# Kernel optimization log

Hardware: AMD Instinct MI355X
Metric: run time of the kernel (lower is better)

Reference implementation:

```python
import jax, jax.numpy as jnp
import numpy as np

B, S, D, H = 2, 2048, 1024, 16
HD = D // H  # head_dim = 64
ROPE_BASE = 10000.0
INIT_STD = 0.02


def setup_inputs() -> dict:
    key = jax.random.key(0)
    k1, k2, k3 = jax.random.split(key, 3)
    x = jax.random.normal(k1, (B, S, D), dtype=jnp.float32)
    w_qkv = jax.random.normal(k2, (3 * D, D), dtype=jnp.float32) * INIT_STD
    w_out = jax.random.normal(k3, (D, D), dtype=jnp.float32) * (1.0 / np.sqrt(D))
    b_out = jnp.zeros((D,), dtype=jnp.float32)
    return {"x": x, "w_qkv": w_qkv, "w_out": w_out, "b_out": b_out}


def _rope_cos_sin(s_len, head_dim, dtype):
    theta = 1.0 / ROPE_BASE ** (jnp.arange(0, head_dim, 2, dtype=jnp.float32) / head_dim)
    freqs = jnp.outer(jnp.arange(s_len, dtype=jnp.float32), theta)  # [s, d/2]
    freqs = jnp.concatenate([freqs, freqs], axis=-1)  # [s, d]
    return jnp.cos(freqs).astype(dtype), jnp.sin(freqs).astype(dtype)


def _apply_rope(qk, cos, sin):
    # qk: [b, h, s, d]; rotate-half: (-x2, x1)
    d2 = qk.shape[-1] // 2
    x1, x2 = qk[..., :d2], qk[..., d2:]
    rot = jnp.concatenate([-x2, x1], axis=-1)
    return qk * cos + rot * sin


def reference(x, w_qkv, w_out, b_out):
    b, s, d = x.shape
    qkv = jnp.einsum('bsd,ed->bse', x, w_qkv)  # [b, s, 3D]
    qkv = qkv.reshape(b, s, 3 * H, HD).transpose(0, 2, 1, 3)  # [b, 3h, s, d]
    qk, v = qkv[:, :2 * H], qkv[:, 2 * H:]
    cos, sin = _rope_cos_sin(s, HD, x.dtype)
    qk = _apply_rope(qk, cos, sin)
    q, k = qk[:, :H], qk[:, H:]
    scale = 1.0 / np.sqrt(HD)
    scores = jnp.einsum('bhqd,bhkd->bhqk', q, k) * scale  # [b, h, s, s]
    causal = jnp.tril(jnp.ones((s, s), dtype=bool))
    scores = jnp.where(causal, scores, jnp.finfo(scores.dtype).min)
    attn = jax.nn.softmax(scores, axis=-1)
    o = jnp.einsum('bhqk,bhkd->bhqd', attn, v)  # [b, h, s, d]
    o = o.transpose(0, 2, 1, 3).reshape(b, s, d)
    return jnp.einsum('bsd,ed->bse', o, w_out) + b_out
```

## Files before the change

### kernel.cpp

```cpp
#include <hip/hip_runtime.h>
#include <hip/hip_fp16.h>
#include <math.h>

#define B_  2
#define S_  2048
#define D_  1024
#define H_  16
#define HD_ 64

typedef _Float16  f16;
typedef __attribute__((ext_vector_type(8))) _Float16 f16x8;
typedef __attribute__((ext_vector_type(4))) _Float16 f16x4;
typedef __attribute__((ext_vector_type(4))) float    f32x4;

#define LOG2E 1.4426950408889634f
#define L2_10000_DIV32 0.41524101186092029f
#define PS 72

__device__ __forceinline__ float fin(float v) { return (v == v) ? v : 0.0f; }

__device__ __forceinline__ f16x8 cvt8(const float* p) {
  float4 a = *(const float4*)p;
  float4 b = *(const float4*)(p + 4);
  f16x8 h;
  h[0] = (f16)a.x; h[1] = (f16)a.y; h[2] = (f16)a.z; h[3] = (f16)a.w;
  h[4] = (f16)b.x; h[5] = (f16)b.y; h[6] = (f16)b.z; h[7] = (f16)b.w;
  return h;
}

__global__ void __launch_bounds__(256)
k_qkv_rope(const float* __restrict__ x, const float* __restrict__ wqkv,
           f16* __restrict__ Qb, f16* __restrict__ Kb, f16* __restrict__ Vt)
{
  __shared__ __align__(16) f16 As[128 * 64];
  __shared__ __align__(16) f16 Bs[128 * 64];
  const int t = threadIdx.x;
  const int w = t >> 6;
  const int lane = t & 63;
  const int ll = lane & 15;
  const int quad = lane >> 4;
  const int wm = w >> 1, wn = w & 1;
  const int row0 = blockIdx.y * 128;
  const int col0 = blockIdx.x * 128;

  const f32x4 fz = {0.f, 0.f, 0.f, 0.f};
  f32x4 acc[4][4];
#pragma unroll
  for (int i = 0; i < 4; ++i)
#pragma unroll
    for (int j = 0; j < 4; ++j) acc[i][j] = fz;

  const int ldr = t >> 3;
  const int ldk = (t & 7) * 8;
  const float* ga = x    + (size_t)(row0 + ldr) * D_ + ldk;
  const float* gb = wqkv + (size_t)(col0 + ldr) * D_ + ldk;

  for (int kt = 0; kt < D_; kt += 64) {
    f16x8 ra[4], rb[4];
#pragma unroll
    for (int i = 0; i < 4; ++i) {
      ra[i] = cvt8(ga + (size_t)i * 32 * D_ + kt);
      rb[i] = cvt8(gb + (size_t)i * 32 * D_ + kt);
    }
    __syncthreads();
#pragma unroll
    for (int i = 0; i < 4; ++i) {
      *(f16x8*)&As[(i * 32 + ldr) * 64 + ldk] = ra[i];
      *(f16x8*)&Bs[(i * 32 + ldr) * 64 + ldk] = rb[i];
    }
    __syncthreads();
#pragma unroll
    for (int kk = 0; kk < 64; kk += 32) {
      f16x8 a[4], b[4];
#pragma unroll
      for (int mt = 0; mt < 4; ++mt)
        a[mt] = *(const f16x8*)&As[(wm * 64 + mt * 16 + ll) * 64 + kk + quad * 8];
#pragma unroll
      for (int nt = 0; nt < 4; ++nt)
        b[nt] = *(const f16x8*)&Bs[(wn * 64 + nt * 16 + ll) * 64 + kk + quad * 8];
#pragma unroll
      for (int mt = 0; mt < 4; ++mt)
#pragma unroll
        for (int nt = 0; nt < 4; ++nt)
          acc[mt][nt] = __builtin_amdgcn_mfma_f32_16x16x32_f16(
              a[mt], b[nt], acc[mt][nt], 0, 0, 0);
    }
  }

  const int h3 = (col0 >> 6) + wn;
  if (h3 < 32) {
    f16* dst = (h3 < 16) ? Qb : Kb;
    const int h = (h3 < 16) ? h3 : h3 - 16;
    const float th0 = exp2f(-(float)ll * L2_10000_DIV32);
    const float th1 = exp2f(-(float)(16 + ll) * L2_10000_DIV32);
#pragma unroll
    for (int mt = 0; mt < 4; ++mt) {
#pragma unroll
      for (int r = 0; r < 4; ++r) {
        const int row = row0 + wm * 64 + mt * 16 + quad * 4 + r;
        const int b = row >> 11;
        const int p = row & (S_ - 1);
        f16* base = dst + ((size_t)(b * H_ + h) * S_ + p) * HD_;
        const float fp = (float)p;
        float s0, c0, s1, c1;
        sincosf(fp * th0, &s0, &c0);
        sincosf(fp * th1, &s1, &c1);
        {
          float x1 = acc[mt][0][r], x2 = acc[mt][2][r];
          base[ll]      = (f16)fin(x1 * c0 - x2 * s0);
          base[ll + 32] = (f16)fin(x2 * c0 + x1 * s0);
        }
        {
          float x1 = acc[mt][1][r], x2 = acc[mt][3][r];
          base[16 + ll]      = (f16)fin(x1 * c1 - x2 * s1);
          base[16 + ll + 32] = (f16)fin(x2 * c1 + x1 * s1);
        }
      }
    }
  } else {
    const int hv = h3 - 32;
#pragma unroll
    for (int mt = 0; mt < 4; ++mt)
#pragma unroll
      for (int nt = 0; nt < 4; ++nt)
#pragma unroll
        for (int r = 0; r < 4; ++r) {
          const int row = row0 + wm * 64 + mt * 16 + quad * 4 + r;
          const int b = row >> 11;
          const int p = row & (S_ - 1);
          const int dd = nt * 16 + ll;
          Vt[((size_t)(b * H_ + hv) * HD_ + dd) * S_ + p] = (f16)fin(acc[mt][nt][r]);
        }
  }
}

__device__ __forceinline__ void softmax_tile(
    f32x4 sc[4], bool diag, int qloc, int ll, int quad,
    float& mrun, float& lrun, float& alpha, f16* Pt)
{
  float pm = -3.0e4f;
#pragma unroll
  for (int nt = 0; nt < 4; ++nt)
#pragma unroll
    for (int r = 0; r < 4; ++r) {
      float s = sc[nt][r];
      s = (s == s) ? s : -3.0e4f;
      if (diag && (nt * 16 + quad * 4 + r) > qloc) s = -3.0e4f;
      sc[nt][r] = s;
      pm = fmaxf(pm, s);
    }
  pm = fmaxf(pm, __shfl_xor(pm, 16));
  pm = fmaxf(pm, __shfl_xor(pm, 32));
  const float mn = fmaxf(mrun, pm);
  alpha = exp2f(mrun - mn);
  mrun = mn;
  float ps = 0.f;
#pragma unroll
  for (int nt = 0; nt < 4; ++nt) {
    f16x4 pk;
#pragma unroll
    for (int r = 0; r < 4; ++r) {
      float p = exp2f(sc[nt][r] - mn);
      ps += p;
      pk[r] = (f16)p;
    }
    *(f16x4*)&Pt[ll * PS + nt * 16 + quad * 4] = pk;
  }
  ps += __shfl_xor(ps, 16);
  ps += __shfl_xor(ps, 32);
  lrun = lrun * alpha + ps;
}

__device__ __forceinline__ void write_o(
    f32x4 acco[4], float lrun, f16* Pt, int ll, int quad, int w,
    int qt, int b, int h, f16* __restrict__ Ob)
{
  const float inv = 1.0f / fmaxf(lrun, 1e-30f);
#pragma unroll
  for (int dg = 0; dg < 4; ++dg) {
    f16x4 ov;
#pragma unroll
    for (int r = 0; r < 4; ++r) ov[r] = (f16)fin(acco[dg][r] * inv);
    *(f16x4*)&Pt[ll * PS + dg * 16 + quad * 4] = ov;
  }
#pragma unroll
  for (int s2 = 0; s2 < 2; ++s2) {
    f16x8 o = *(const f16x8*)&Pt[ll * PS + (quad + 4 * s2) * 8];
    const size_t row = (size_t)b * S_ + qt * 64 + w * 16 + ll;
    *(f16x8*)&Ob[row * D_ + h * HD_ + (quad + 4 * s2) * 8] = o;
  }
}

__global__ void __launch_bounds__(256, 2)
k_attn2(const f16* __restrict__ Qb, const f16* __restrict__ Kb,
        const f16* __restrict__ Vt, f16* __restrict__ Ob)
{
  __shared__ __align__(16) f16 Qs[128 * PS];
  __shared__ __align__(16) f16 Ks[2][64 * PS];
  __shared__ __align__(16) f16 Vs[2][64 * PS];
  __shared__ __align__(16) f16 Ps[4][16 * PS];

  const int t = threadIdx.x;
  const int w = t >> 6;
  const int lane = t & 63;
  const int ll = lane & 15;
  const int quad = lane >> 4;
  const int qtA = blockIdx.x;
  const int qtB = 31 - qtA;
  const int h = blockIdx.y;
  const int b = blockIdx.z;
  const size_t bh = (size_t)b * H_ + h;
  const f16* Qg = Qb + bh * S_ * HD_;
  const f16* Kg = Kb + bh * S_ * HD_;
  const f16* Vg = Vt + bh * HD_ * S_;

  {
    const int r = t >> 1;
    const int c0 = (t & 1) * 32;
    const int grow = (r < 64) ? (qtA * 64 + r) : (qtB * 64 + r - 64);
    const f16 hsc = (f16)(0.125f * LOG2E);
#pragma unroll
    for (int j = 0; j < 4; ++j) {
      f16x8 v = *(const f16x8*)(Qg + (size_t)grow * HD_ + c0 + j * 8);
#pragma unroll
      for (int e = 0; e < 8; ++e) v[e] *= hsc;
      *(f16x8*)&Qs[r * PS + c0 + j * 8] = v;
    }
  }
  {
    const int r = t >> 2;
    const int c = (t & 3) * 16;
    f16x8 a0 = *(const f16x8*)(Kg + (size_t)r * HD_ + c);
    f16x8 a1 = *(const f16x8*)(Kg + (size_t)r * HD_ + c + 8);
    f16x8 b0 = *(const f16x8*)(Vg + (size_t)r * S_ + c);
    f16x8 b1 = *(const f16x8*)(Vg + (size_t)r * S_ + c + 8);
    *(f16x8*)&Ks[0][r * PS + c]     = a0;
    *(f16x8*)&Ks[0][r * PS + c + 8] = a1;
    *(f16x8*)&Vs[0][r * PS + c]     = b0;
    *(f16x8*)&Vs[0][r * PS + c + 8] = b1;
  }
  __syncthreads();

  const f32x4 fz = {0.f, 0.f, 0.f, 0.f};
  f32x4 accoA[4], accoB[4];
#pragma unroll
  for (int i = 0; i < 4; ++i) { accoA[i] = fz; accoB[i] = fz; }
  float mA = -3.0e4f, lA = 0.f, mB = -3.0e4f, lB = 0.f;
  const int qloc = w * 16 + ll;
  f16* Pt = &Ps[w][0];

  for (int kt = 0; kt <= qtB; ++kt) {
    const int cur = kt & 1;
    const bool pre = (kt < qtB);
    const int sr = t >> 2, scc = (t & 3) * 16;
    f16x8 nk0, nk1, nv0, nv1;
    if (pre) {
      const int kn = (kt + 1) * 64;
      nk0 = *(const f16x8*)(Kg + (size_t)(kn + sr) * HD_ + scc);
      nk1 = *(const f16x8*)(Kg + (size_t)(kn + sr) * HD_ + scc + 8);
      nv0 = *(const f16x8*)(Vg + (size_t)sr * S_ + kn + scc);
      nv1 = *(const f16x8*)(Vg + (size_t)sr * S_ + kn + scc + 8);
    }
    const f16* Kc = Ks[cur];
    const f16* Vc = Vs[cur];
    const bool doA = (kt <= qtA);

    f16x8 ak[2][4];
#pragma unroll
    for (int k2 = 0; k2 < 2; ++k2)
#pragma unroll
      for (int nt = 0; nt < 4; ++nt)
        ak[k2][nt] = *(const f16x8*)&Kc[(nt * 16 + ll) * PS + k2 * 32 + quad * 8];

    f32x4 sB[4] = {fz, fz, fz, fz};
#pragma unroll
    for (int k2 = 0; k2 < 2; ++k2) {
      f16x8 bq = *(const f16x8*)&Qs[(64 + w * 16 + ll) * PS + k2 * 32 + quad * 8];
#pragma unroll
      for (int nt = 0; nt < 4; ++nt)
        sB[nt] = __builtin_amdgcn_mfma_f32_16x16x32_f16(ak[k2][nt], bq, sB[nt], 0, 0, 0);
    }
    f32x4 sA[4] = {fz, fz, fz, fz};
    if (doA) {
#pragma unroll
      for (int k2 = 0; k2 < 2; ++k2) {
        f16x8 bq = *(const f16x8*)&Qs[(w * 16 + ll) * PS + k2 * 32 + quad * 8];
#pragma unroll
        for (int nt = 0; nt < 4; ++nt)
          sA[nt] = __builtin_amdgcn_mfma_f32_16x16x32_f16(ak[k2][nt], bq, sA[nt], 0, 0, 0);
      }
    }

    f16x8 av[2][4];
#pragma unroll
    for (int k2 = 0; k2 < 2; ++k2)
#pragma unroll
      for (int dg = 0; dg < 4; ++dg)
        av[k2][dg] = *(const f16x8*)&Vc[(dg * 16 + ll) * PS + k2 * 32 + quad * 8];

    float alpha;
    if (doA) {
      softmax_tile(sA, kt == qtA, qloc, ll, quad, mA, lA, alpha, Pt);
#pragma unroll
      for (int dg = 0; dg < 4; ++dg)
#pragma unroll
        for (int r = 0; r < 4; ++r) accoA[dg][r] *= alpha;
#pragma unroll
      for (int k2 = 0; k2 < 2; ++k2) {
        f16x8 bp = *(const f16x8*)&Pt[ll * PS + k2 * 32 + quad * 8];
#pragma unroll
        for (int dg = 0; dg < 4; ++dg)
          accoA[dg] = __builtin_amdgcn_mfma_f32_16x16x32_f16(av[k2][dg], bp, accoA[dg], 0, 0, 0);
      }
    }
    {
      softmax_tile(sB, kt == qtB, qloc, ll, quad, mB, lB, alpha, Pt);
#pragma unroll
      for (int dg = 0; dg < 4; ++dg)
#pragma unroll
        for (int r = 0; r < 4; ++r) accoB[dg][r] *= alpha;
#pragma unroll
      for (int k2 = 0; k2 < 2; ++k2) {
        f16x8 bp = *(const f16x8*)&Pt[ll * PS + k2 * 32 + quad * 8];
#pragma unroll
        for (int dg = 0; dg < 4; ++dg)
          accoB[dg] = __builtin_amdgcn_mfma_f32_16x16x32_f16(av[k2][dg], bp, accoB[dg], 0, 0, 0);
      }
    }

    if (pre) {
      *(f16x8*)&Ks[1 - cur][sr * PS + scc]     = nk0;
      *(f16x8*)&Ks[1 - cur][sr * PS + scc + 8] = nk1;
      *(f16x8*)&Vs[1 - cur][sr * PS + scc]     = nv0;
      *(f16x8*)&Vs[1 - cur][sr * PS + scc + 8] = nv1;
    }
    __syncthreads();
  }

  write_o(accoA, lA, Pt, ll, quad, w, qtA, b, h, Ob);
  write_o(accoB, lB, Pt, ll, quad, w, qtB, b, h, Ob);
}

__global__ void __launch_bounds__(256)
k_out_main(const f16* __restrict__ A, const float* __restrict__ W,
           const float* __restrict__ bias, float* __restrict__ out)
{
  __shared__ __align__(16) f16 As[128 * 64];
  __shared__ __align__(16) f16 Bs[128 * 64];
  const int t = threadIdx.x;
  const int w = t >> 6;
  const int lane = t & 63;
  const int ll = lane & 15;
  const int quad = lane >> 4;
  const int wm = w >> 1, wn = w & 1;
  const int row0 = blockIdx.y * 128;
  const int col0 = blockIdx.x * 128;

  const f32x4 fz = {0.f, 0.f, 0.f, 0.f};
  f32x4 acc[4][4];
#pragma unroll
  for (int i = 0; i < 4; ++i)
#pragma unroll
    for (int j = 0; j < 4; ++j) acc[i][j] = fz;

  const int ldr = t >> 3;
  const int ldk = (t & 7) * 8;
  const f16*   ga = A + (size_t)(row0 + ldr) * D_ + ldk;
  const float* gb = W + (size_t)(col0 + ldr) * D_ + ldk;

  for (int kt = 0; kt < D_; kt += 64) {
    f16x8 ra[4], rb[4];
#pragma unroll
    for (int i = 0; i < 4; ++i) {
      ra[i] = *(const f16x8*)(ga + (size_t)i * 32 * D_ + kt);
      rb[i] = cvt8(gb + (size_t)i * 32 * D_ + kt);
    }
    __syncthreads();
#pragma unroll
    for (int i = 0; i < 4; ++i) {
      *(f16x8*)&As[(i * 32 + ldr) * 64 + ldk] = ra[i];
      *(f16x8*)&Bs[(i * 32 + ldr) * 64 + ldk] = rb[i];
    }
    __syncthreads();
#pragma unroll
    for (int kk = 0; kk < 64; kk += 32) {
      f16x8 a[4], b[4];
#pragma unroll
      for (int mt = 0; mt < 4; ++mt)
        a[mt] = *(const f16x8*)&As[(wm * 64 + mt * 16 + ll) * 64 + kk + quad * 8];
#pragma unroll
      for (int nt = 0; nt < 4; ++nt)
        b[nt] = *(const f16x8*)&Bs[(wn * 64 + nt * 16 + ll) * 64 + kk + quad * 8];
#pragma unroll
      for (int mt = 0; mt < 4; ++mt)
#pragma unroll
        for (int nt = 0; nt < 4; ++nt)
          acc[mt][nt] = __builtin_amdgcn_mfma_f32_16x16x32_f16(
              a[mt], b[nt], acc[mt][nt], 0, 0, 0);
    }
  }

#pragma unroll
  for (int mt = 0; mt < 4; ++mt)
#pragma unroll
    for (int r = 0; r < 4; ++r) {
      const int row = row0 + wm * 64 + mt * 16 + quad * 4 + r;
#pragma unroll
      for (int nt = 0; nt < 4; ++nt) {
        const int col = col0 + wn * 64 + nt * 16 + ll;
        out[(size_t)row * D_ + col] = fin(acc[mt][nt][r] + bias[col]);
      }
    }
}

extern "C" void kernel_launch(void* const* d_in, const int* in_sizes, int n_in,
                              void* d_out, int out_size, void* d_ws, size_t ws_size,
                              hipStream_t stream) {
  const float* x    = (const float*)d_in[0];
  const float* wqkv = (const float*)d_in[1];
  const float* wout = (const float*)d_in[2];
  const float* bout = (const float*)d_in[3];
  float* out = (float*)d_out;

  char* ws = (char*)d_ws;
  f16* Qb = (f16*)(ws);
  f16* Kb = (f16*)(ws + ((size_t)8  << 20));
  f16* Vt = (f16*)(ws + ((size_t)16 << 20));
  f16* Ob = (f16*)(ws + ((size_t)24 << 20));

  k_qkv_rope<<<dim3(3 * D_ / 128, (B_ * S_) / 128), 256, 0, stream>>>(
      x, wqkv, Qb, Kb, Vt);
  k_attn2<<<dim3(16, H_, B_), 256, 0, stream>>>(Qb, Kb, Vt, Ob);
  k_out_main<<<dim3(D_ / 128, (B_ * S_) / 128), 256, 0, stream>>>(
      Ob, wout, bout, out);
}
```

Baseline: 215.8 us.

## Pre-convert weights and x to fp16 and stage GEMM tiles via global_load_lds

Adds a conversion kernel that casts w_qkv, w_out and optionally x to fp16 in the workspace. The QKV and output GEMMs then load tiles straight into LDS with global_load_lds, removing per-tile fp32 conversion and register staging. Attention output is written in place over Q in a head-major layout, and the output GEMM reads that layout directly. This costs an extra launch and a full conversion pass over the weights on every call, adds a second barrier per k-step, and aliases the attention output with its Q input.

```diff
diff --git a/kernel.cpp b/kernel.cpp
--- a/kernel.cpp
+++ b/kernel.cpp
@@ -28,8 +28,35 @@
   return h;
 }
 
+__device__ __forceinline__ void gload16(const f16* g, f16* l) {
+  __builtin_amdgcn_global_load_lds(
+      (__attribute__((address_space(1))) void*)(const_cast<f16*>(g)),
+      (__attribute__((address_space(3))) void*)l, 16, 0, 0);
+}
+
 __global__ void __launch_bounds__(256)
-k_qkv_rope(const float* __restrict__ x, const float* __restrict__ wqkv,
+k_cvt3(const float* __restrict__ wq, const float* __restrict__ wo,
+       const float* __restrict__ x,
+       f16* __restrict__ wqh, f16* __restrict__ woh, f16* __restrict__ xh,
+       int doX)
+{
+  const int NWQ = 3 * D_ * D_ / 4, NWO = D_ * D_ / 4, NX = B_ * S_ * D_ / 4;
+  const int n = NWQ + NWO + (doX ? NX : 0);
+  for (int i = blockIdx.x * 256 + threadIdx.x; i < n; i += gridDim.x * 256) {
+    const float* src; f16* dst; int j;
+    if (i < NWQ)            { src = wq; dst = wqh; j = i; }
+    else if (i < NWQ + NWO) { src = wo; dst = woh; j = i - NWQ; }
+    else                    { src = x;  dst = xh;  j = i - NWQ - NWO; }
+    float4 v = ((const float4*)src)[j];
+    f16x4 h = {(f16)v.x, (f16)v.y, (f16)v.z, (f16)v.w};
+    ((f16x4*)dst)[j] = h;
+  }
+}
+
+template <bool XF16>
+__global__ void __launch_bounds__(256)
+k_qkv_rope(const float* __restrict__ xf, const f16* __restrict__ xh,
+           const f16* __restrict__ wqh,
            f16* __restrict__ Qb, f16* __restrict__ Kb, f16* __restrict__ Vt)
 {
   __shared__ __align__(16) f16 As[128 * 64];
@@ -52,21 +79,23 @@
 
   const int ldr = t >> 3;
   const int ldk = (t & 7) * 8;
-  const float* ga = x    + (size_t)(row0 + ldr) * D_ + ldk;
-  const float* gb = wqkv + (size_t)(col0 + ldr) * D_ + ldk;
+  const float* gaf = xf  + (size_t)(row0 + ldr) * D_ + ldk;
+  const f16*   gah = xh  + (size_t)(row0 + ldr) * D_ + ldk;
+  const f16*   gb  = wqh + (size_t)(col0 + ldr) * D_ + ldk;
 
   for (int kt = 0; kt < D_; kt += 64) {
-    f16x8 ra[4], rb[4];
 #pragma unroll
     for (int i = 0; i < 4; ++i) {
-      ra[i] = cvt8(ga + (size_t)i * 32 * D_ + kt);
-      rb[i] = cvt8(gb + (size_t)i * 32 * D_ + kt);
-    }
-    __syncthreads();
-#pragma unroll
-    for (int i = 0; i < 4; ++i) {
-      *(f16x8*)&As[(i * 32 + ldr) * 64 + ldk] = ra[i];
-      *(f16x8*)&Bs[(i * 32 + ldr) * 64 + ldk] = rb[i];
+      gload16(gb + (size_t)i * 32 * D_ + kt, &Bs[(i * 32 + w * 8) * 64]);
+      if (XF16) gload16(gah + (size_t)i * 32 * D_ + kt, &As[(i * 32 + w * 8) * 64]);
+    }
+    if (!XF16) {
+      f16x8 ra[4];
+#pragma unroll
+      for (int i = 0; i < 4; ++i) ra[i] = cvt8(gaf + (size_t)i * 32 * D_ + kt);
+#pragma unroll
+      for (int i = 0; i < 4; ++i)
+        *(f16x8*)&As[(i * 32 + ldr) * 64 + ldk] = ra[i];
     }
     __syncthreads();
 #pragma unroll
@@ -85,6 +114,7 @@
           acc[mt][nt] = __builtin_amdgcn_mfma_f32_16x16x32_f16(
               a[mt], b[nt], acc[mt][nt], 0, 0, 0);
     }
+    __syncthreads();
   }
 
   const int h3 = (col0 >> 6) + wn;
@@ -173,7 +203,7 @@
 
 __device__ __forceinline__ void write_o(
     f32x4 acco[4], float lrun, f16* Pt, int ll, int quad, int w,
-    int qt, int b, int h, f16* __restrict__ Ob)
+    int qt, size_t bh, f16* Ob)
 {
   const float inv = 1.0f / fmaxf(lrun, 1e-30f);
 #pragma unroll
@@ -186,14 +216,14 @@
 #pragma unroll
   for (int s2 = 0; s2 < 2; ++s2) {
     f16x8 o = *(const f16x8*)&Pt[ll * PS + (quad + 4 * s2) * 8];
-    const size_t row = (size_t)b * S_ + qt * 64 + w * 16 + ll;
-    *(f16x8*)&Ob[row * D_ + h * HD_ + (quad + 4 * s2) * 8] = o;
+    const size_t row = bh * S_ + qt * 64 + w * 16 + ll;
+    *(f16x8*)&Ob[row * HD_ + (quad + 4 * s2) * 8] = o;
   }
 }
 
 __global__ void __launch_bounds__(256, 2)
-k_attn2(const f16* __restrict__ Qb, const f16* __restrict__ Kb,
-        const f16* __restrict__ Vt, f16* __restrict__ Ob)
+k_attn2(const f16* Qb, const f16* __restrict__ Kb,
+        const f16* __restrict__ Vt, f16* Ob)
 {
   __shared__ __align__(16) f16 Qs[128 * PS];
   __shared__ __align__(16) f16 Ks[2][64 * PS];
@@ -337,12 +367,12 @@
     __syncthreads();
   }
 
-  write_o(accoA, lA, Pt, ll, quad, w, qtA, b, h, Ob);
-  write_o(accoB, lB, Pt, ll, quad, w, qtB, b, h, Ob);
+  write_o(accoA, lA, Pt, ll, quad, w, qtA, bh, Ob);
+  write_o(accoB, lB, Pt, ll, quad, w, qtB, bh, Ob);
 }
 
 __global__ void __launch_bounds__(256)
-k_out_main(const f16* __restrict__ A, const float* __restrict__ W,
+k_out_main(const f16* __restrict__ Ob, const f16* __restrict__ Wh,
            const float* __restrict__ bias, float* __restrict__ out)
 {
   __shared__ __align__(16) f16 As[128 * 64];
@@ -355,6 +385,8 @@
   const int wm = w >> 1, wn = w & 1;
   const int row0 = blockIdx.y * 128;
   const int col0 = blockIdx.x * 128;
+  const int bb = row0 >> 11;
+  const int s0 = row0 & (S_ - 1);
 
   const f32x4 fz = {0.f, 0.f, 0.f, 0.f};
   f32x4 acc[4][4];
@@ -365,21 +397,15 @@
 
   const int ldr = t >> 3;
   const int ldk = (t & 7) * 8;
-  const f16*   ga = A + (size_t)(row0 + ldr) * D_ + ldk;
-  const float* gb = W + (size_t)(col0 + ldr) * D_ + ldk;
+  const f16* gb = Wh + (size_t)(col0 + ldr) * D_ + ldk;
 
   for (int kt = 0; kt < D_; kt += 64) {
-    f16x8 ra[4], rb[4];
+    const int hh = kt >> 6;
+    const f16* ga = Ob + (((size_t)(bb * H_ + hh)) * S_ + s0 + ldr) * HD_ + ldk;
 #pragma unroll
     for (int i = 0; i < 4; ++i) {
-      ra[i] = *(const f16x8*)(ga + (size_t)i * 32 * D_ + kt);
-      rb[i] = cvt8(gb + (size_t)i * 32 * D_ + kt);
-    }
-    __syncthreads();
-#pragma unroll
-    for (int i = 0; i < 4; ++i) {
-      *(f16x8*)&As[(i * 32 + ldr) * 64 + ldk] = ra[i];
-      *(f16x8*)&Bs[(i * 32 + ldr) * 64 + ldk] = rb[i];
+      gload16(ga + (size_t)i * 32 * HD_, &As[(i * 32 + w * 8) * 64]);
+      gload16(gb + (size_t)i * 32 * D_ + kt, &Bs[(i * 32 + w * 8) * 64]);
     }
     __syncthreads();
 #pragma unroll
@@ -398,6 +424,7 @@
           acc[mt][nt] = __builtin_amdgcn_mfma_f32_16x16x32_f16(
               a[mt], b[nt], acc[mt][nt], 0, 0, 0);
     }
+    __syncthreads();
   }
 
 #pragma unroll
@@ -423,14 +450,22 @@
   float* out = (float*)d_out;
 
   char* ws = (char*)d_ws;
-  f16* Qb = (f16*)(ws);
-  f16* Kb = (f16*)(ws + ((size_t)8  << 20));
-  f16* Vt = (f16*)(ws + ((size_t)16 << 20));
-  f16* Ob = (f16*)(ws + ((size_t)24 << 20));
-
-  k_qkv_rope<<<dim3(3 * D_ / 128, (B_ * S_) / 128), 256, 0, stream>>>(
-      x, wqkv, Qb, Kb, Vt);
-  k_attn2<<<dim3(16, H_, B_), 256, 0, stream>>>(Qb, Kb, Vt, Ob);
+  f16* wqh = (f16*)(ws);
+  f16* Qb  = (f16*)(ws + 6291456);
+  f16* Kb  = (f16*)(ws + 14680064);
+  f16* Vt  = (f16*)(ws + 23068672);
+  f16* woh = (f16*)(ws + 31457280);
+  const bool bigws = ws_size >= (size_t)41943040;
+  f16* xh  = (f16*)(ws + 33554432);
+
+  k_cvt3<<<2048, 256, 0, stream>>>(wqkv, wout, x, wqh, woh, xh, bigws ? 1 : 0);
+  if (bigws)
+    k_qkv_rope<true><<<dim3(3 * D_ / 128, (B_ * S_) / 128), 256, 0, stream>>>(
+        x, xh, wqh, Qb, Kb, Vt);
+  else
+    k_qkv_rope<false><<<dim3(3 * D_ / 128, (B_ * S_) / 128), 256, 0, stream>>>(
+        x, xh, wqh, Qb, Kb, Vt);
+  k_attn2<<<dim3(16, H_, B_), 256, 0, stream>>>(Qb, Kb, Vt, Qb );
   k_out_main<<<dim3(D_ / 128, (B_ * S_) / 128), 256, 0, stream>>>(
-      Ob, wout, bout, out);
-}
+      Qb, woh, bout, out);
+}
```

Result: no change. 216.4 us (+0.3%).
